# Performance work log

Hardware: AMD Instinct MI355X
Metric: run time of the kernel (lower is better)

Reference implementation:

```python
import jax, jax.numpy as jnp
import numpy as np

B, F, H, M, T = 4096, 256, 256, 3, 30
IN0 = 2 + F  # GRU layer-0 input: concat(current_pos[2], context[F])


def setup_inputs() -> dict:
    key = jax.random.key(0)
    ks = jax.random.split(key, 15)
    s = 0.05
    rn = lambda k, shp: jax.random.normal(k, shp, jnp.float32) * s
    return dict(
        context=jax.random.normal(ks[0], (B, F), jnp.float32),
        mp_w1=rn(ks[1], (64, F)), mp_b1=rn(ks[2], (64,)),
        mp_w2=rn(ks[3], (M, 64)), mp_b2=rn(ks[4], (M,)),
        w_ih0=rn(ks[5], (M, 3 * H, IN0)), w_hh0=rn(ks[6], (M, 3 * H, H)),
        b_ih0=rn(ks[7], (M, 3 * H)), b_hh0=rn(ks[8], (M, 3 * H)),
        w_ih1=rn(ks[9], (M, 3 * H, H)), w_hh1=rn(ks[10], (M, 3 * H, H)),
        b_ih1=rn(ks[11], (M, 3 * H)), b_hh1=rn(ks[12], (M, 3 * H)),
        out_w=rn(ks[13], (M, 2, H)), out_b=rn(ks[14], (M, 2)),
        num_future_steps=T,
    )


def _gru_cell(x, h, w_ih, w_hh, b_ih, b_hh):
    # PyTorch GRU cell, gate order (r, z, n)
    gx = x @ w_ih.T + b_ih  # (B, 3H)
    gh = h @ w_hh.T + b_hh  # (B, 3H)
    xr, xz, xn = jnp.split(gx, 3, axis=-1)
    hr, hz, hn = jnp.split(gh, 3, axis=-1)
    r = jax.nn.sigmoid(xr + hr)
    z = jax.nn.sigmoid(xz + hz)
    n = jnp.tanh(xn + r * hn)
    return (1.0 - z) * n + z * h


def reference(context, mp_w1, mp_b1, mp_w2, mp_b2,
              w_ih0, w_hh0, b_ih0, b_hh0,
              w_ih1, w_hh1, b_ih1, b_hh1,
              out_w, out_b, num_future_steps):
    mode_logits = jax.nn.relu(context @ mp_w1.T + mp_b1) @ mp_w2.T + mp_b2
    mode_probs = jax.nn.softmax(mode_logits, axis=-1)  # (B, M)

    def decode_mode(wi0, wh0, bi0, bh0, wi1, wh1, bi1, bh1, ow, ob):
        def step(carry, _):
            h0, h1, pos = carry
            x = jnp.concatenate([pos, context], axis=-1)  # (B, 2+F)
            h0n = _gru_cell(x, h0, wi0, wh0, bi0, bh0)
            h1n = _gru_cell(h0n, h1, wi1, wh1, bi1, bh1)
            delta = h1n @ ow.T + ob  # (B, 2)
            return (h0n, h1n, delta), delta

        pos0 = jnp.zeros((context.shape[0], 2), context.dtype)
        # hidden = context.unsqueeze(0).repeat(2,1,1): both layers init to context
        (_, _, _), deltas = jax.lax.scan(step, (context, context, pos0), None,
                                          length=num_future_steps)
        # deltas: (T, B, 2) -> (B, T, 2), cumulative sum over time
        return jnp.cumsum(deltas.transpose(1, 0, 2), axis=1)

    trajs = jax.vmap(decode_mode)(w_ih0, w_hh0, b_ih0, b_hh0,
                                  w_ih1, w_hh1, b_ih1, b_hh1,
                                  out_w, out_b)  # (M, B, T, 2)
    trajectories = trajs.transpose(1, 0, 2, 3)  # (B, M, T, 2)
    return trajectories, mode_probs
```

## Files before the change

kernel.cpp:

```cpp
#include <hip/hip_runtime.h>


typedef __attribute__((ext_vector_type(8))) short bf16x8;
typedef __attribute__((ext_vector_type(4))) float f32x4;

__device__ __forceinline__ short f2bf(float f) {
    unsigned u = __builtin_bit_cast(unsigned, f);
    unsigned r = (u + 0x7fffu + ((u >> 16) & 1u)) >> 16;
    return (short)r;
}
__device__ __forceinline__ float bf2f(short s) {
    unsigned u = ((unsigned)(unsigned short)s) << 16;
    return __builtin_bit_cast(float, u);
}
__device__ __forceinline__ float fast_sigmoid(float x) {
    x = fminf(fmaxf(x, -30.f), 30.f);
    float e = __builtin_amdgcn_exp2f(x * -1.442695041f);
    return __builtin_amdgcn_rcpf(1.f + e);
}
__device__ __forceinline__ float fast_tanh(float x) {
    x = fminf(fmaxf(x, -15.f), 15.f);
    float e = __builtin_amdgcn_exp2f(x * -2.885390082f);
    return (1.f - e) * __builtin_amdgcn_rcpf(1.f + e);
}

__global__ void prep_kernel(const float* __restrict__ w_ih0,
                            const float* __restrict__ w_hh0,
                            const float* __restrict__ w_ih1,
                            const float* __restrict__ w_hh1,
                            short* __restrict__ ws) {
    int bid = blockIdx.x;
    int L = threadIdx.x;
    const float* src;
    int srcRowLen, colBase, m, w, ks, t;
    if (bid < 1152) {
        int idx = bid, mw = idx / 48, blk = idx % 48;
        m = mw / 8; w = mw % 8;
        if (blk < 32) { ks = blk >> 2; t = blk & 3; }
        else { int q = blk - 32; ks = q >> 1; t = 4 + (q & 1); }
        src = w_hh0 + (size_t)m * 768 * 256; srcRowLen = 256; colBase = 0;
    } else if (bid < 3456) {
        int idx = bid - 1152, mw = idx / 96, blk = idx % 96;
        m = mw / 8; w = mw % 8;
        int half;
        if (blk < 64) { half = blk >> 5; ks = (blk >> 2) & 7; t = blk & 3; }
        else { int q = blk - 64; half = q >> 4; ks = (q >> 1) & 7; t = 4 + (q & 1); }
        src = (half ? w_hh1 : w_ih1) + (size_t)m * 768 * 256;
        srcRowLen = 256; colBase = 0;
    } else {
        int idx = bid - 3456, mw = idx / 48, blk = idx % 48;
        m = mw / 8; w = mw % 8; ks = blk / 6; t = blk % 6;
        src = w_ih0 + (size_t)m * 768 * 258; srcRowLen = 258; colBase = 2;
    }
    int row = (t >> 1) * 256 + 32 * w + (t & 1) * 16 + (L & 15);
    int col0 = colBase + ks * 32 + (L >> 4) * 8;
    short* dst = ws + (size_t)bid * 512 + L * 8;
    const float* s = src + (size_t)row * srcRowLen + col0;
#pragma unroll
    for (int j = 0; j < 8; ++j) dst[j] = f2bf(s[j]);
}

__global__ __launch_bounds__(256) void modeprobs_kernel(
    const float* __restrict__ ctx, const float* __restrict__ w1,
    const float* __restrict__ b1, const float* __restrict__ w2,
    const float* __restrict__ b2, float* __restrict__ out,
    long probs_off) {
    __shared__ float w1s[64 * 256];
    int tid = threadIdx.x;
    int j = tid & 63;
    int rsub = tid >> 6;
#pragma unroll
    for (int i = 0; i < 64; ++i) w1s[tid + i * 256] = w1[tid + i * 256];
    float b1v = b1[j];
    float w2v0 = w2[j], w2v1 = w2[64 + j], w2v2 = w2[128 + j];
    float b20 = b2[0], b21 = b2[1], b22 = b2[2];
    __syncthreads();
    for (int c = 0; c < 16; ++c) {
        int brow = blockIdx.x * 64 + c * 4 + rsub;
        const float* crow = ctx + (size_t)brow * 256;
        float accv = b1v;
#pragma unroll 8
        for (int k = 0; k < 256; ++k) {
            int kk = (k + j) & 255;
            accv += w1s[j * 256 + kk] * crow[kk];
        }
        float h = fmaxf(accv, 0.f);
        float l0 = h * w2v0, l1 = h * w2v1, l2 = h * w2v2;
#pragma unroll
        for (int s = 1; s < 64; s <<= 1) {
            l0 += __shfl_xor(l0, s);
            l1 += __shfl_xor(l1, s);
            l2 += __shfl_xor(l2, s);
        }
        if (j == 0) {
            l0 += b20; l1 += b21; l2 += b22;
            float mx = fmaxf(l0, fmaxf(l1, l2));
            float e0 = __builtin_amdgcn_exp2f((l0 - mx) * 1.442695041f);
            float e1 = __builtin_amdgcn_exp2f((l1 - mx) * 1.442695041f);
            float e2 = __builtin_amdgcn_exp2f((l2 - mx) * 1.442695041f);
            float inv = 1.f / (e0 + e1 + e2);
            out[probs_off + (size_t)brow * 3 + 0] = e0 * inv;
            out[probs_off + (size_t)brow * 3 + 1] = e1 * inv;
            out[probs_off + (size_t)brow * 3 + 2] = e2 * inv;
        }
    }
}

__global__ __launch_bounds__(512, 2) void decoder_kernel(
    const float* __restrict__ context,
    const float* __restrict__ w_ih0_f,
    const float* __restrict__ b_ih0, const float* __restrict__ b_hh0,
    const float* __restrict__ b_ih1, const float* __restrict__ b_hh1,
    const float* __restrict__ out_w, const float* __restrict__ out_b,
    const short* __restrict__ ws, float* __restrict__ out,
    const int* __restrict__ pT, int ntiles) {
    __shared__ short ctxS[64 * 264];
    __shared__ short h0a[64 * 264], h0b[64 * 264];
    __shared__ short h1s[64 * 264];
    __shared__ float posD[128];
    __shared__ float owl[512];
    __shared__ float cwp0[768], cwp1[768];
    __shared__ float cbA[512];
    __shared__ float cbXn[256];
    __shared__ float cbh0n[256];
    __shared__ float cb1A[512];
    __shared__ float cb1X[256];
    __shared__ float cb1H[256];

    const int bid = blockIdx.x;
    const int xcd = bid & 7, slot = bid >> 3;
    int mode, xl, nx;
    if (xcd < 3)      { mode = 0; xl = xcd;     nx = 3; }
    else if (xcd < 6) { mode = 1; xl = xcd - 3; nx = 3; }
    else              { mode = 2; xl = xcd - 6; nx = 2; }
    const int g = slot * nx + xl;
    if (g >= ntiles) return;
    const int m = mode;
    const int b0 = g * 64;

    const int T = *pT;
    const int tid = threadIdx.x;
    const int lane = tid & 63, w = tid >> 6;
    const int lr = lane & 15, quad = lane >> 4;

    if (tid < 128) posD[tid] = 0.f;
    owl[tid] = out_w[m * 512 + tid];
    if (tid < 512) {
        cbA[tid] = b_ih0[m * 768 + tid] + b_hh0[m * 768 + tid];
        cb1A[tid] = b_ih1[m * 768 + tid] + b_hh1[m * 768 + tid];
    }
    if (tid < 256) {
        cbXn[tid] = b_ih0[m * 768 + 512 + tid];
        cbh0n[tid] = b_hh0[m * 768 + 512 + tid];
        cb1X[tid] = b_ih1[m * 768 + 512 + tid];
        cb1H[tid] = b_hh1[m * 768 + 512 + tid];
    }
    for (int c = tid; c < 768; c += 512) {
        cwp0[c] = w_ih0_f[((size_t)m * 768 + c) * 258 + 0];
        cwp1[c] = w_ih0_f[((size_t)m * 768 + c) * 258 + 1];
    }
#pragma unroll
    for (int i = 0; i < 32; ++i) {
        int idx = tid + i * 512;
        int r = idx >> 8, k = idx & 255;
        short v = f2bf(context[(size_t)(b0 + r) * 256 + k]);
        ctxS[r * 264 + k] = v;
        h0a[r * 264 + k] = v;
        h1s[r * 264 + k] = v;
    }
    const float ob0v = out_b[m * 2 + 0], ob1v = out_b[m * 2 + 1];

    const short* p0w = ws + ((size_t)(m * 8 + w) * 48) * 512 + lane * 8;
    const short* p1w = ws + (size_t)1152 * 512 + ((size_t)(m * 8 + w) * 96) * 512 + lane * 8;
    const short* pcw = ws + (size_t)3456 * 512 + ((size_t)(m * 8 + w) * 48) * 512 + lane * 8;

    const int cA = 32 * w + lr;
    const int cB = 32 * w + 16 + lr;

    __syncthreads();

    float cum0 = 0.f, cum1 = 0.f;

    for (int st = 0; st < T; ++st) {
        const short* h0c = (st & 1) ? h0b : h0a;
        short* h0n_ = (st & 1) ? h0a : h0b;

        {
            f32x4 arz[4][4], axn[2][4], ahn[2][4];
#pragma unroll
            for (int rt = 0; rt < 4; ++rt)
#pragma unroll
                for (int r = 0; r < 4; ++r) {
                    int row = rt * 16 + quad * 4 + r;
                    float px = posD[row * 2], py = posD[row * 2 + 1];
#pragma unroll
                    for (int t = 0; t < 4; ++t) {
                        int c = (t >> 1) * 256 + ((t & 1) ? cB : cA);
                        arz[t][rt][r] = cbA[c] + px * cwp0[c] + py * cwp1[c];
                    }
#pragma unroll
                    for (int nt = 0; nt < 2; ++nt) {
                        int cn = nt ? cB : cA;
                        axn[nt][rt][r] = cbXn[cn] + px * cwp0[512 + cn] +
                                         py * cwp1[512 + cn];
                        ahn[nt][rt][r] = cbh0n[cn];
                    }
                }
            const short* bpc = pcw;
            const short* bp0rz = p0w;
            const short* bp0n = p0w + 32 * 512;
#pragma unroll 1
            for (int ks = 0; ks < 8; ++ks) {
                bf16x8 ac[4], ah[4];
#pragma unroll
                for (int rt = 0; rt < 4; ++rt) {
                    ac[rt] = *reinterpret_cast<const bf16x8*>(
                        ctxS + (rt * 16 + lr) * 264 + ks * 32 + quad * 8);
                    ah[rt] = *reinterpret_cast<const bf16x8*>(
                        h0c + (rt * 16 + lr) * 264 + ks * 32 + quad * 8);
                }
#pragma unroll
                for (int t = 0; t < 4; ++t) {
                    bf16x8 b = *reinterpret_cast<const bf16x8*>(bpc + t * 512);
#pragma unroll
                    for (int rt = 0; rt < 4; ++rt)
                        arz[t][rt] = __builtin_amdgcn_mfma_f32_16x16x32_bf16(
                            ac[rt], b, arz[t][rt], 0, 0, 0);
                }
#pragma unroll
                for (int nt = 0; nt < 2; ++nt) {
                    bf16x8 b = *reinterpret_cast<const bf16x8*>(bpc + (4 + nt) * 512);
#pragma unroll
                    for (int rt = 0; rt < 4; ++rt)
                        axn[nt][rt] = __builtin_amdgcn_mfma_f32_16x16x32_bf16(
                            ac[rt], b, axn[nt][rt], 0, 0, 0);
                }
#pragma unroll
                for (int t = 0; t < 4; ++t) {
                    bf16x8 b = *reinterpret_cast<const bf16x8*>(bp0rz + t * 512);
#pragma unroll
                    for (int rt = 0; rt < 4; ++rt)
                        arz[t][rt] = __builtin_amdgcn_mfma_f32_16x16x32_bf16(
                            ah[rt], b, arz[t][rt], 0, 0, 0);
                }
#pragma unroll
                for (int nt = 0; nt < 2; ++nt) {
                    bf16x8 b = *reinterpret_cast<const bf16x8*>(bp0n + nt * 512);
#pragma unroll
                    for (int rt = 0; rt < 4; ++rt)
                        ahn[nt][rt] = __builtin_amdgcn_mfma_f32_16x16x32_bf16(
                            ah[rt], b, ahn[nt][rt], 0, 0, 0);
                }
                bpc += 6 * 512;
                bp0rz += 4 * 512;
                bp0n += 2 * 512;
            }
#pragma unroll
            for (int nt = 0; nt < 2; ++nt) {
                int col = nt ? cB : cA;
#pragma unroll
                for (int rt = 0; rt < 4; ++rt)
#pragma unroll
                    for (int r = 0; r < 4; ++r) {
                        int row = rt * 16 + quad * 4 + r;
                        float rr = fast_sigmoid(arz[nt][rt][r]);
                        float zz = fast_sigmoid(arz[2 + nt][rt][r]);
                        float nn =
                            fast_tanh(axn[nt][rt][r] + rr * ahn[nt][rt][r]);
                        float hold = bf2f(h0c[row * 264 + col]);
                        h0n_[row * 264 + col] = f2bf((1.f - zz) * nn + zz * hold);
                    }
            }
        }
        __syncthreads();

        {
            f32x4 arz[4][4], axn[2][4], ahn[2][4];
#pragma unroll
            for (int rt = 0; rt < 4; ++rt)
#pragma unroll
                for (int r = 0; r < 4; ++r) {
#pragma unroll
                    for (int t = 0; t < 4; ++t) {
                        int c = (t >> 1) * 256 + ((t & 1) ? cB : cA);
                        arz[t][rt][r] = cb1A[c];
                    }
#pragma unroll
                    for (int nt = 0; nt < 2; ++nt) {
                        int cn = nt ? cB : cA;
                        axn[nt][rt][r] = cb1X[cn];
                        ahn[nt][rt][r] = cb1H[cn];
                    }
                }
            const short* bq0 = p1w;
            const short* bq1 = p1w + 32 * 512;
            const short* bx = p1w + 64 * 512;
            const short* bh = p1w + 80 * 512;
#pragma unroll 1
            for (int ks = 0; ks < 8; ++ks) {
                bf16x8 a0[4], a1[4];
#pragma unroll
                for (int rt = 0; rt < 4; ++rt) {
                    a0[rt] = *reinterpret_cast<const bf16x8*>(
                        h0n_ + (rt * 16 + lr) * 264 + ks * 32 + quad * 8);
                    a1[rt] = *reinterpret_cast<const bf16x8*>(
                        h1s + (rt * 16 + lr) * 264 + ks * 32 + quad * 8);
                }
#pragma unroll
                for (int t = 0; t < 4; ++t) {
                    bf16x8 b = *reinterpret_cast<const bf16x8*>(bq0 + t * 512);
#pragma unroll
                    for (int rt = 0; rt < 4; ++rt)
                        arz[t][rt] = __builtin_amdgcn_mfma_f32_16x16x32_bf16(
                            a0[rt], b, arz[t][rt], 0, 0, 0);
                }
#pragma unroll
                for (int nt = 0; nt < 2; ++nt) {
                    bf16x8 b = *reinterpret_cast<const bf16x8*>(bx + nt * 512);
#pragma unroll
                    for (int rt = 0; rt < 4; ++rt)
                        axn[nt][rt] = __builtin_amdgcn_mfma_f32_16x16x32_bf16(
                            a0[rt], b, axn[nt][rt], 0, 0, 0);
                }
#pragma unroll
                for (int t = 0; t < 4; ++t) {
                    bf16x8 b = *reinterpret_cast<const bf16x8*>(bq1 + t * 512);
#pragma unroll
                    for (int rt = 0; rt < 4; ++rt)
                        arz[t][rt] = __builtin_amdgcn_mfma_f32_16x16x32_bf16(
                            a1[rt], b, arz[t][rt], 0, 0, 0);
                }
#pragma unroll
                for (int nt = 0; nt < 2; ++nt) {
                    bf16x8 b = *reinterpret_cast<const bf16x8*>(bh + nt * 512);
#pragma unroll
                    for (int rt = 0; rt < 4; ++rt)
                        ahn[nt][rt] = __builtin_amdgcn_mfma_f32_16x16x32_bf16(
                            a1[rt], b, ahn[nt][rt], 0, 0, 0);
                }
                bq0 += 4 * 512;
                bq1 += 4 * 512;
                bx += 2 * 512;
                bh += 2 * 512;
            }
            __syncthreads();
#pragma unroll
            for (int nt = 0; nt < 2; ++nt) {
                int col = nt ? cB : cA;
#pragma unroll
                for (int rt = 0; rt < 4; ++rt)
#pragma unroll
                    for (int r = 0; r < 4; ++r) {
                        int row = rt * 16 + quad * 4 + r;
                        float rr = fast_sigmoid(arz[nt][rt][r]);
                        float zz = fast_sigmoid(arz[2 + nt][rt][r]);
                        float nn =
                            fast_tanh(axn[nt][rt][r] + rr * ahn[nt][rt][r]);
                        float hold = bf2f(h1s[row * 264 + col]);
                        h1s[row * 264 + col] = f2bf((1.f - zz) * nn + zz * hold);
                    }
            }
        }
        __syncthreads();

        {
            int brow = tid >> 3, p = tid & 7;
            float d0 = 0.f, d1 = 0.f;
#pragma unroll
            for (int j = 0; j < 4; ++j) {
                int cb = ((p + brow) & 7) * 8 + j * 64;
                bf16x8 hv8 = *reinterpret_cast<const bf16x8*>(h1s + brow * 264 + cb);
#pragma unroll
                for (int i = 0; i < 8; ++i) {
                    float hv = bf2f(hv8[i]);
                    d0 += hv * owl[cb + i];
                    d1 += hv * owl[256 + cb + i];
                }
            }
            d0 += __shfl_xor(d0, 1); d0 += __shfl_xor(d0, 2); d0 += __shfl_xor(d0, 4);
            d1 += __shfl_xor(d1, 1); d1 += __shfl_xor(d1, 2); d1 += __shfl_xor(d1, 4);
            d0 += ob0v;
            d1 += ob1v;
            if (p == 0) {
                cum0 += d0;
                cum1 += d1;
                size_t o = (((size_t)(b0 + brow) * 3 + m) * (size_t)T + st) * 2;
                out[o] = cum0;
                out[o + 1] = cum1;
                posD[brow * 2] = d0;
                posD[brow * 2 + 1] = d1;
            }
        }
        __syncthreads();
    }
}

extern "C" void kernel_launch(void* const* d_in, const int* in_sizes, int n_in,
                              void* d_out, int out_size, void* d_ws, size_t ws_size,
                              hipStream_t stream) {
    const float* context = (const float*)d_in[0];
    const float* mp_w1 = (const float*)d_in[1];
    const float* mp_b1 = (const float*)d_in[2];
    const float* mp_w2 = (const float*)d_in[3];
    const float* mp_b2 = (const float*)d_in[4];
    const float* w_ih0 = (const float*)d_in[5];
    const float* w_hh0 = (const float*)d_in[6];
    const float* b_ih0 = (const float*)d_in[7];
    const float* b_hh0 = (const float*)d_in[8];
    const float* w_ih1 = (const float*)d_in[9];
    const float* w_hh1 = (const float*)d_in[10];
    const float* b_ih1 = (const float*)d_in[11];
    const float* b_hh1 = (const float*)d_in[12];
    const float* out_w = (const float*)d_in[13];
    const float* out_b = (const float*)d_in[14];
    const int* pT = (const int*)d_in[15];
    float* out = (float*)d_out;
    short* ws = (short*)d_ws;

    const int B = in_sizes[0] / 256;
    const int ntiles = B / 64;
    const long probs_off = (long)out_size - (long)B * 3;

    prep_kernel<<<4608, 64, 0, stream>>>(w_ih0, w_hh0, w_ih1, w_hh1, ws);
    modeprobs_kernel<<<B / 64, 256, 0, stream>>>(context, mp_w1, mp_b1, mp_w2,
                                                 mp_b2, out, probs_off);
    const int nslots = (ntiles + 1) / 2;
    decoder_kernel<<<8 * nslots, 512, 0, stream>>>(
        context, w_ih0, b_ih0, b_hh0, b_ih1, b_hh1, out_w, out_b, ws, out, pT,
        ntiles);
}
```

Baseline: 976.4 us.

## Switch GRU recurrent GEMMs from 16x16x32 to 32x32x16 bf16 MFMA tiles

Replaces the 16x16x32 MFMA tiling of both GRU layers with 32x32x16 MFMA, where each wave covers a 32-column slice with two 64-row tiles. The prep kernel re-packs the bf16 weight fragments to match the new operand layout. The gate epilogues and bias initialisation are rewritten for the 32x32 accumulator register mapping. The aim is fewer MFMA instructions and fewer LDS A-operand loads per unit of work, in exchange for a new fragment layout and different register pressure.

```diff
diff --git a/kernel.cpp b/kernel.cpp
--- a/kernel.cpp
+++ b/kernel.cpp
@@ -2,7 +2,7 @@
 
 
 typedef __attribute__((ext_vector_type(8))) short bf16x8;
-typedef __attribute__((ext_vector_type(4))) float f32x4;
+typedef __attribute__((ext_vector_type(16))) float f32x16;
 
 __device__ __forceinline__ short f2bf(float f) {
     unsigned u = __builtin_bit_cast(unsigned, f);
@@ -32,28 +32,32 @@
     int bid = blockIdx.x;
     int L = threadIdx.x;
     const float* src;
-    int srcRowLen, colBase, m, w, ks, t;
+    int srcRowLen, colBase, m, w, ks, gb;
     if (bid < 1152) {
         int idx = bid, mw = idx / 48, blk = idx % 48;
         m = mw / 8; w = mw % 8;
-        if (blk < 32) { ks = blk >> 2; t = blk & 3; }
-        else { int q = blk - 32; ks = q >> 1; t = 4 + (q & 1); }
+        if (blk < 32) { ks = blk >> 1; gb = (blk & 1) * 256; }
+        else { ks = blk - 32; gb = 512; }
         src = w_hh0 + (size_t)m * 768 * 256; srcRowLen = 256; colBase = 0;
     } else if (bid < 3456) {
         int idx = bid - 1152, mw = idx / 96, blk = idx % 96;
         m = mw / 8; w = mw % 8;
         int half;
-        if (blk < 64) { half = blk >> 5; ks = (blk >> 2) & 7; t = blk & 3; }
-        else { int q = blk - 64; half = q >> 4; ks = (q >> 1) & 7; t = 4 + (q & 1); }
+        if (blk < 32)      { half = 0; ks = blk >> 1;        gb = (blk & 1) * 256; }
+        else if (blk < 64) { half = 1; ks = (blk - 32) >> 1; gb = (blk & 1) * 256; }
+        else if (blk < 80) { half = 0; ks = blk - 64;        gb = 512; }
+        else               { half = 1; ks = blk - 80;        gb = 512; }
         src = (half ? w_hh1 : w_ih1) + (size_t)m * 768 * 256;
         srcRowLen = 256; colBase = 0;
     } else {
         int idx = bid - 3456, mw = idx / 48, blk = idx % 48;
-        m = mw / 8; w = mw % 8; ks = blk / 6; t = blk % 6;
+        m = mw / 8; w = mw % 8;
+        if (blk < 32) { ks = blk >> 1; gb = (blk & 1) * 256; }
+        else { ks = blk - 32; gb = 512; }
         src = w_ih0 + (size_t)m * 768 * 258; srcRowLen = 258; colBase = 2;
     }
-    int row = (t >> 1) * 256 + 32 * w + (t & 1) * 16 + (L & 15);
-    int col0 = colBase + ks * 32 + (L >> 4) * 8;
+    int row = gb + 32 * w + (L & 31);
+    int col0 = colBase + ks * 16 + (L >> 5) * 8;
     short* dst = ws + (size_t)bid * 512 + L * 8;
     const float* s = src + (size_t)row * srcRowLen + col0;
 #pragma unroll
@@ -141,7 +145,8 @@
     const int T = *pT;
     const int tid = threadIdx.x;
     const int lane = tid & 63, w = tid >> 6;
-    const int lr = lane & 15, quad = lane >> 4;
+    const int l31 = lane & 31, lhi = lane >> 5;
+    const int c = 32 * w + l31;
 
     if (tid < 128) posD[tid] = 0.f;
     owl[tid] = out_w[m * 512 + tid];
@@ -155,9 +160,9 @@
         cb1X[tid] = b_ih1[m * 768 + 512 + tid];
         cb1H[tid] = b_hh1[m * 768 + 512 + tid];
     }
-    for (int c = tid; c < 768; c += 512) {
-        cwp0[c] = w_ih0_f[((size_t)m * 768 + c) * 258 + 0];
-        cwp1[c] = w_ih0_f[((size_t)m * 768 + c) * 258 + 1];
+    for (int cc = tid; cc < 768; cc += 512) {
+        cwp0[cc] = w_ih0_f[((size_t)m * 768 + cc) * 258 + 0];
+        cwp1[cc] = w_ih0_f[((size_t)m * 768 + cc) * 258 + 1];
     }
 #pragma unroll
     for (int i = 0; i < 32; ++i) {
@@ -174,9 +179,6 @@
     const short* p1w = ws + (size_t)1152 * 512 + ((size_t)(m * 8 + w) * 96) * 512 + lane * 8;
     const short* pcw = ws + (size_t)3456 * 512 + ((size_t)(m * 8 + w) * 48) * 512 + lane * 8;
 
-    const int cA = 32 * w + lr;
-    const int cB = 32 * w + 16 + lr;
-
     __syncthreads();
 
     float cum0 = 0.f, cum1 = 0.f;
@@ -186,180 +188,169 @@
         short* h0n_ = (st & 1) ? h0a : h0b;
 
         {
-            f32x4 arz[4][4], axn[2][4], ahn[2][4];
-#pragma unroll
-            for (int rt = 0; rt < 4; ++rt)
-#pragma unroll
-                for (int r = 0; r < 4; ++r) {
-                    int row = rt * 16 + quad * 4 + r;
-                    float px = posD[row * 2], py = posD[row * 2 + 1];
-#pragma unroll
-                    for (int t = 0; t < 4; ++t) {
-                        int c = (t >> 1) * 256 + ((t & 1) ? cB : cA);
-                        arz[t][rt][r] = cbA[c] + px * cwp0[c] + py * cwp1[c];
+            f32x16 arz[2][2], axn[2], ahn[2];
+            const float bAr = cbA[c], bAz = cbA[256 + c];
+            const float bXnv = cbXn[c], bh0nv = cbh0n[c];
+            const float w0r = cwp0[c], w1r = cwp1[c];
+            const float w0z = cwp0[256 + c], w1z = cwp1[256 + c];
+            const float w0n = cwp0[512 + c], w1n = cwp1[512 + c];
+#pragma unroll
+            for (int rt = 0; rt < 2; ++rt)
+#pragma unroll
+                for (int gq = 0; gq < 4; ++gq)
+#pragma unroll
+                    for (int q = 0; q < 4; ++q) {
+                        int reg = gq * 4 + q;
+                        int row = rt * 32 + q + 8 * gq + 4 * lhi;
+                        float px = posD[row * 2], py = posD[row * 2 + 1];
+                        arz[0][rt][reg] = bAr + px * w0r + py * w1r;
+                        arz[1][rt][reg] = bAz + px * w0z + py * w1z;
+                        axn[rt][reg] = bXnv + px * w0n + py * w1n;
+                        ahn[rt][reg] = bh0nv;
                     }
-#pragma unroll
-                    for (int nt = 0; nt < 2; ++nt) {
-                        int cn = nt ? cB : cA;
-                        axn[nt][rt][r] = cbXn[cn] + px * cwp0[512 + cn] +
-                                         py * cwp1[512 + cn];
-                        ahn[nt][rt][r] = cbh0n[cn];
+            const short* bcr = pcw;
+            const short* bcn = pcw + 32 * 512;
+            const short* b0r = p0w;
+            const short* b0n = p0w + 32 * 512;
+#pragma unroll 1
+            for (int ks = 0; ks < 16; ++ks) {
+                bf16x8 ac[2], ah[2];
+#pragma unroll
+                for (int rt = 0; rt < 2; ++rt) {
+                    ac[rt] = *reinterpret_cast<const bf16x8*>(
+                        ctxS + (rt * 32 + l31) * 264 + ks * 16 + lhi * 8);
+                    ah[rt] = *reinterpret_cast<const bf16x8*>(
+                        h0c + (rt * 32 + l31) * 264 + ks * 16 + lhi * 8);
+                }
+#pragma unroll
+                for (int t = 0; t < 2; ++t) {
+                    bf16x8 b = *reinterpret_cast<const bf16x8*>(bcr + t * 512);
+#pragma unroll
+                    for (int rt = 0; rt < 2; ++rt)
+                        arz[t][rt] = __builtin_amdgcn_mfma_f32_32x32x16_bf16(
+                            ac[rt], b, arz[t][rt], 0, 0, 0);
+                }
+                {
+                    bf16x8 b = *reinterpret_cast<const bf16x8*>(bcn);
+#pragma unroll
+                    for (int rt = 0; rt < 2; ++rt)
+                        axn[rt] = __builtin_amdgcn_mfma_f32_32x32x16_bf16(
+                            ac[rt], b, axn[rt], 0, 0, 0);
+                }
+#pragma unroll
+                for (int t = 0; t < 2; ++t) {
+                    bf16x8 b = *reinterpret_cast<const bf16x8*>(b0r + t * 512);
+#pragma unroll
+                    for (int rt = 0; rt < 2; ++rt)
+                        arz[t][rt] = __builtin_amdgcn_mfma_f32_32x32x16_bf16(
+                            ah[rt], b, arz[t][rt], 0, 0, 0);
+                }
+                {
+                    bf16x8 b = *reinterpret_cast<const bf16x8*>(b0n);
+#pragma unroll
+                    for (int rt = 0; rt < 2; ++rt)
+                        ahn[rt] = __builtin_amdgcn_mfma_f32_32x32x16_bf16(
+                            ah[rt], b, ahn[rt], 0, 0, 0);
+                }
+                bcr += 2 * 512;
+                bcn += 512;
+                b0r += 2 * 512;
+                b0n += 512;
+            }
+#pragma unroll
+            for (int rt = 0; rt < 2; ++rt)
+#pragma unroll
+                for (int gq = 0; gq < 4; ++gq)
+#pragma unroll
+                    for (int q = 0; q < 4; ++q) {
+                        int reg = gq * 4 + q;
+                        int row = rt * 32 + q + 8 * gq + 4 * lhi;
+                        float rr = fast_sigmoid(arz[0][rt][reg]);
+                        float zz = fast_sigmoid(arz[1][rt][reg]);
+                        float nn = fast_tanh(axn[rt][reg] + rr * ahn[rt][reg]);
+                        float hold = bf2f(h0c[row * 264 + c]);
+                        h0n_[row * 264 + c] = f2bf((1.f - zz) * nn + zz * hold);
                     }
-                }
-            const short* bpc = pcw;
-            const short* bp0rz = p0w;
-            const short* bp0n = p0w + 32 * 512;
-#pragma unroll 1
-            for (int ks = 0; ks < 8; ++ks) {
-                bf16x8 ac[4], ah[4];
-#pragma unroll
-                for (int rt = 0; rt < 4; ++rt) {
-                    ac[rt] = *reinterpret_cast<const bf16x8*>(
-                        ctxS + (rt * 16 + lr) * 264 + ks * 32 + quad * 8);
-                    ah[rt] = *reinterpret_cast<const bf16x8*>(
-                        h0c + (rt * 16 + lr) * 264 + ks * 32 + quad * 8);
-                }
-#pragma unroll
-                for (int t = 0; t < 4; ++t) {
-                    bf16x8 b = *reinterpret_cast<const bf16x8*>(bpc + t * 512);
-#pragma unroll
-                    for (int rt = 0; rt < 4; ++rt)
-                        arz[t][rt] = __builtin_amdgcn_mfma_f32_16x16x32_bf16(
-                            ac[rt], b, arz[t][rt], 0, 0, 0);
-                }
-#pragma unroll
-                for (int nt = 0; nt < 2; ++nt) {
-                    bf16x8 b = *reinterpret_cast<const bf16x8*>(bpc + (4 + nt) * 512);
-#pragma unroll
-                    for (int rt = 0; rt < 4; ++rt)
-                        axn[nt][rt] = __builtin_amdgcn_mfma_f32_16x16x32_bf16(
-                            ac[rt], b, axn[nt][rt], 0, 0, 0);
-                }
-#pragma unroll
-                for (int t = 0; t < 4; ++t) {
-                    bf16x8 b = *reinterpret_cast<const bf16x8*>(bp0rz + t * 512);
-#pragma unroll
-                    for (int rt = 0; rt < 4; ++rt)
-                        arz[t][rt] = __builtin_amdgcn_mfma_f32_16x16x32_bf16(
-                            ah[rt], b, arz[t][rt], 0, 0, 0);
-                }
-#pragma unroll
-                for (int nt = 0; nt < 2; ++nt) {
-                    bf16x8 b = *reinterpret_cast<const bf16x8*>(bp0n + nt * 512);
-#pragma unroll
-                    for (int rt = 0; rt < 4; ++rt)
-                        ahn[nt][rt] = __builtin_amdgcn_mfma_f32_16x16x32_bf16(
-                            ah[rt], b, ahn[nt][rt], 0, 0, 0);
-                }
-                bpc += 6 * 512;
-                bp0rz += 4 * 512;
-                bp0n += 2 * 512;
-            }
-#pragma unroll
-            for (int nt = 0; nt < 2; ++nt) {
-                int col = nt ? cB : cA;
-#pragma unroll
-                for (int rt = 0; rt < 4; ++rt)
-#pragma unroll
-                    for (int r = 0; r < 4; ++r) {
-                        int row = rt * 16 + quad * 4 + r;
-                        float rr = fast_sigmoid(arz[nt][rt][r]);
-                        float zz = fast_sigmoid(arz[2 + nt][rt][r]);
-                        float nn =
-                            fast_tanh(axn[nt][rt][r] + rr * ahn[nt][rt][r]);
-                        float hold = bf2f(h0c[row * 264 + col]);
-                        h0n_[row * 264 + col] = f2bf((1.f - zz) * nn + zz * hold);
-                    }
-            }
         }
         __syncthreads();
 
         {
-            f32x4 arz[4][4], axn[2][4], ahn[2][4];
-#pragma unroll
-            for (int rt = 0; rt < 4; ++rt)
-#pragma unroll
-                for (int r = 0; r < 4; ++r) {
-#pragma unroll
-                    for (int t = 0; t < 4; ++t) {
-                        int c = (t >> 1) * 256 + ((t & 1) ? cB : cA);
-                        arz[t][rt][r] = cb1A[c];
-                    }
-#pragma unroll
-                    for (int nt = 0; nt < 2; ++nt) {
-                        int cn = nt ? cB : cA;
-                        axn[nt][rt][r] = cb1X[cn];
-                        ahn[nt][rt][r] = cb1H[cn];
-                    }
+            f32x16 arz[2][2], axn[2], ahn[2];
+            const float bAr = cb1A[c], bAz = cb1A[256 + c];
+            const float bXv = cb1X[c], bHv = cb1H[c];
+#pragma unroll
+            for (int rt = 0; rt < 2; ++rt)
+#pragma unroll
+                for (int reg = 0; reg < 16; ++reg) {
+                    arz[0][rt][reg] = bAr;
+                    arz[1][rt][reg] = bAz;
+                    axn[rt][reg] = bXv;
+                    ahn[rt][reg] = bHv;
                 }
             const short* bq0 = p1w;
             const short* bq1 = p1w + 32 * 512;
             const short* bx = p1w + 64 * 512;
             const short* bh = p1w + 80 * 512;
 #pragma unroll 1
-            for (int ks = 0; ks < 8; ++ks) {
-                bf16x8 a0[4], a1[4];
-#pragma unroll
-                for (int rt = 0; rt < 4; ++rt) {
+            for (int ks = 0; ks < 16; ++ks) {
+                bf16x8 a0[2], a1[2];
+#pragma unroll
+                for (int rt = 0; rt < 2; ++rt) {
                     a0[rt] = *reinterpret_cast<const bf16x8*>(
-                        h0n_ + (rt * 16 + lr) * 264 + ks * 32 + quad * 8);
+                        h0n_ + (rt * 32 + l31) * 264 + ks * 16 + lhi * 8);
                     a1[rt] = *reinterpret_cast<const bf16x8*>(
-                        h1s + (rt * 16 + lr) * 264 + ks * 32 + quad * 8);
-                }
-#pragma unroll
-                for (int t = 0; t < 4; ++t) {
+                        h1s + (rt * 32 + l31) * 264 + ks * 16 + lhi * 8);
+                }
+#pragma unroll
+                for (int t = 0; t < 2; ++t) {
                     bf16x8 b = *reinterpret_cast<const bf16x8*>(bq0 + t * 512);
 #pragma unroll
-                    for (int rt = 0; rt < 4; ++rt)
-                        arz[t][rt] = __builtin_amdgcn_mfma_f32_16x16x32_bf16(
+                    for (int rt = 0; rt < 2; ++rt)
+                        arz[t][rt] = __builtin_amdgcn_mfma_f32_32x32x16_bf16(
                             a0[rt], b, arz[t][rt], 0, 0, 0);
                 }
-#pragma unroll
-                for (int nt = 0; nt < 2; ++nt) {
-                    bf16x8 b = *reinterpret_cast<const bf16x8*>(bx + nt * 512);
-#pragma unroll
-                    for (int rt = 0; rt < 4; ++rt)
-                        axn[nt][rt] = __builtin_amdgcn_mfma_f32_16x16x32_bf16(
-                            a0[rt], b, axn[nt][rt], 0, 0, 0);
-                }
-#pragma unroll
-                for (int t = 0; t < 4; ++t) {
+                {
+                    bf16x8 b = *reinterpret_cast<const bf16x8*>(bx);
+#pragma unroll
+                    for (int rt = 0; rt < 2; ++rt)
+                        axn[rt] = __builtin_amdgcn_mfma_f32_32x32x16_bf16(
+                            a0[rt], b, axn[rt], 0, 0, 0);
+                }
+#pragma unroll
+                for (int t = 0; t < 2; ++t) {
                     bf16x8 b = *reinterpret_cast<const bf16x8*>(bq1 + t * 512);
 #pragma unroll
-                    for (int rt = 0; rt < 4; ++rt)
-                        arz[t][rt] = __builtin_amdgcn_mfma_f32_16x16x32_bf16(
+                    for (int rt = 0; rt < 2; ++rt)
+                        arz[t][rt] = __builtin_amdgcn_mfma_f32_32x32x16_bf16(
                             a1[rt], b, arz[t][rt], 0, 0, 0);
                 }
-#pragma unroll
-                for (int nt = 0; nt < 2; ++nt) {
-                    bf16x8 b = *reinterpret_cast<const bf16x8*>(bh + nt * 512);
-#pragma unroll
-                    for (int rt = 0; rt < 4; ++rt)
-                        ahn[nt][rt] = __builtin_amdgcn_mfma_f32_16x16x32_bf16(
-                            a1[rt], b, ahn[nt][rt], 0, 0, 0);
-                }
-                bq0 += 4 * 512;
-                bq1 += 4 * 512;
-                bx += 2 * 512;
-                bh += 2 * 512;
+                {
+                    bf16x8 b = *reinterpret_cast<const bf16x8*>(bh);
+#pragma unroll
+                    for (int rt = 0; rt < 2; ++rt)
+                        ahn[rt] = __builtin_amdgcn_mfma_f32_32x32x16_bf16(
+                            a1[rt], b, ahn[rt], 0, 0, 0);
+                }
+                bq0 += 2 * 512;
+                bq1 += 2 * 512;
+                bx += 512;
+                bh += 512;
             }
             __syncthreads();
 #pragma unroll
-            for (int nt = 0; nt < 2; ++nt) {
-                int col = nt ? cB : cA;
-#pragma unroll
-                for (int rt = 0; rt < 4; ++rt)
-#pragma unroll
-                    for (int r = 0; r < 4; ++r) {
-                        int row = rt * 16 + quad * 4 + r;
-                        float rr = fast_sigmoid(arz[nt][rt][r]);
-                        float zz = fast_sigmoid(arz[2 + nt][rt][r]);
-                        float nn =
-                            fast_tanh(axn[nt][rt][r] + rr * ahn[nt][rt][r]);
-                        float hold = bf2f(h1s[row * 264 + col]);
-                        h1s[row * 264 + col] = f2bf((1.f - zz) * nn + zz * hold);
+            for (int rt = 0; rt < 2; ++rt)
+#pragma unroll
+                for (int gq = 0; gq < 4; ++gq)
+#pragma unroll
+                    for (int q = 0; q < 4; ++q) {
+                        int reg = gq * 4 + q;
+                        int row = rt * 32 + q + 8 * gq + 4 * lhi;
+                        float rr = fast_sigmoid(arz[0][rt][reg]);
+                        float zz = fast_sigmoid(arz[1][rt][reg]);
+                        float nn = fast_tanh(axn[rt][reg] + rr * ahn[rt][reg]);
+                        float hold = bf2f(h1s[row * 264 + c]);
+                        h1s[row * 264 + c] = f2bf((1.f - zz) * nn + zz * hold);
                     }
-            }
         }
         __syncthreads();
 
```

Measured after the change: 1.113 ms. 1.14x slower.

## Halve decoder tile to 32 rows with 256-thread blocks and rebalanced work map

Applied to the files above, without the earlier changes.

The decoder now processes 32-row batch tiles with 4 waves per block instead of 64 rows with 8 waves. Each wave covers two 32-column groups, so per-wave weight loads are reused across fewer rows. Work items are spread across the mode/tile space with a per-XCD contiguous split instead of the fixed 3/3/2 mode-to-XCD mapping. The pos-projection weights are stored in shared memory as bf16. The goal is more blocks and better occupancy and load balance across CUs, at the cost of each weight fragment read from global/L2 being reused over half as many rows, which raises weight traffic.

```diff
diff --git a/kernel.cpp b/kernel.cpp
--- a/kernel.cpp
+++ b/kernel.cpp
@@ -106,20 +106,20 @@
     }
 }
 
-__global__ __launch_bounds__(512, 2) void decoder_kernel(
+__global__ __launch_bounds__(256, 2) void decoder_kernel(
     const float* __restrict__ context,
     const float* __restrict__ w_ih0_f,
     const float* __restrict__ b_ih0, const float* __restrict__ b_hh0,
     const float* __restrict__ b_ih1, const float* __restrict__ b_hh1,
     const float* __restrict__ out_w, const float* __restrict__ out_b,
     const short* __restrict__ ws, float* __restrict__ out,
-    const int* __restrict__ pT, int ntiles) {
-    __shared__ short ctxS[64 * 264];
-    __shared__ short h0a[64 * 264], h0b[64 * 264];
-    __shared__ short h1s[64 * 264];
-    __shared__ float posD[128];
+    const int* __restrict__ pT, int tilesPerMode, int nwork) {
+    __shared__ short ctxS[32 * 264];
+    __shared__ short h0a[32 * 264], h0b[32 * 264];
+    __shared__ short h1s[32 * 264];
+    __shared__ float posD[64];
     __shared__ float owl[512];
-    __shared__ float cwp0[768], cwp1[768];
+    __shared__ short cwp0h[768], cwp1h[768];
     __shared__ float cbA[512];
     __shared__ float cbXn[256];
     __shared__ float cbh0n[256];
@@ -127,55 +127,57 @@
     __shared__ float cb1X[256];
     __shared__ float cb1H[256];
 
-    const int bid = blockIdx.x;
-    const int xcd = bid & 7, slot = bid >> 3;
-    int mode, xl, nx;
-    if (xcd < 3)      { mode = 0; xl = xcd;     nx = 3; }
-    else if (xcd < 6) { mode = 1; xl = xcd - 3; nx = 3; }
-    else              { mode = 2; xl = xcd - 6; nx = 2; }
-    const int g = slot * nx + xl;
-    if (g >= ntiles) return;
-    const int m = mode;
-    const int b0 = g * 64;
+    const int lane8 = blockIdx.x & 7, slot = blockIdx.x >> 3;
+    const int q = nwork >> 3, r8 = nwork & 7;
+    int start, cnt;
+    if (lane8 < r8) { cnt = q + 1; start = lane8 * (q + 1); }
+    else            { cnt = q;     start = r8 * (q + 1) + (lane8 - r8) * q; }
+    if (slot >= cnt) return;
+    const int work = start + slot;
+    const int m = work / tilesPerMode;
+    const int b0 = (work - m * tilesPerMode) * 32;
 
     const int T = *pT;
     const int tid = threadIdx.x;
     const int lane = tid & 63, w = tid >> 6;
     const int lr = lane & 15, quad = lane >> 4;
 
-    if (tid < 128) posD[tid] = 0.f;
+    if (tid < 64) posD[tid] = 0.f;
     owl[tid] = out_w[m * 512 + tid];
-    if (tid < 512) {
-        cbA[tid] = b_ih0[m * 768 + tid] + b_hh0[m * 768 + tid];
-        cb1A[tid] = b_ih1[m * 768 + tid] + b_hh1[m * 768 + tid];
-    }
-    if (tid < 256) {
-        cbXn[tid] = b_ih0[m * 768 + 512 + tid];
-        cbh0n[tid] = b_hh0[m * 768 + 512 + tid];
-        cb1X[tid] = b_ih1[m * 768 + 512 + tid];
-        cb1H[tid] = b_hh1[m * 768 + 512 + tid];
-    }
-    for (int c = tid; c < 768; c += 512) {
-        cwp0[c] = w_ih0_f[((size_t)m * 768 + c) * 258 + 0];
-        cwp1[c] = w_ih0_f[((size_t)m * 768 + c) * 258 + 1];
+    owl[256 + tid] = out_w[m * 512 + 256 + tid];
+    cbA[tid] = b_ih0[m * 768 + tid] + b_hh0[m * 768 + tid];
+    cbA[256 + tid] = b_ih0[m * 768 + 256 + tid] + b_hh0[m * 768 + 256 + tid];
+    cb1A[tid] = b_ih1[m * 768 + tid] + b_hh1[m * 768 + tid];
+    cb1A[256 + tid] = b_ih1[m * 768 + 256 + tid] + b_hh1[m * 768 + 256 + tid];
+    cbXn[tid] = b_ih0[m * 768 + 512 + tid];
+    cbh0n[tid] = b_hh0[m * 768 + 512 + tid];
+    cb1X[tid] = b_ih1[m * 768 + 512 + tid];
+    cb1H[tid] = b_hh1[m * 768 + 512 + tid];
+    for (int cc = tid; cc < 768; cc += 256) {
+        cwp0h[cc] = f2bf(w_ih0_f[((size_t)m * 768 + cc) * 258 + 0]);
+        cwp1h[cc] = f2bf(w_ih0_f[((size_t)m * 768 + cc) * 258 + 1]);
     }
 #pragma unroll
     for (int i = 0; i < 32; ++i) {
-        int idx = tid + i * 512;
-        int r = idx >> 8, k = idx & 255;
-        short v = f2bf(context[(size_t)(b0 + r) * 256 + k]);
-        ctxS[r * 264 + k] = v;
-        h0a[r * 264 + k] = v;
-        h1s[r * 264 + k] = v;
+        int idx = tid + i * 256;
+        int rr = idx >> 8, k = idx & 255;
+        short v = f2bf(context[(size_t)(b0 + rr) * 256 + k]);
+        ctxS[rr * 264 + k] = v;
+        h0a[rr * 264 + k] = v;
+        h1s[rr * 264 + k] = v;
     }
     const float ob0v = out_b[m * 2 + 0], ob1v = out_b[m * 2 + 1];
 
-    const short* p0w = ws + ((size_t)(m * 8 + w) * 48) * 512 + lane * 8;
-    const short* p1w = ws + (size_t)1152 * 512 + ((size_t)(m * 8 + w) * 96) * 512 + lane * 8;
-    const short* pcw = ws + (size_t)3456 * 512 + ((size_t)(m * 8 + w) * 48) * 512 + lane * 8;
-
-    const int cA = 32 * w + lr;
-    const int cB = 32 * w + 16 + lr;
+    const short* p0B[2];
+    const short* p1B[2];
+    const short* pcB[2];
+#pragma unroll
+    for (int g2 = 0; g2 < 2; ++g2) {
+        const int wg = 2 * w + g2;
+        p0B[g2] = ws + ((size_t)(m * 8 + wg) * 48) * 512 + lane * 8;
+        p1B[g2] = ws + (size_t)1152 * 512 + ((size_t)(m * 8 + wg) * 96) * 512 + lane * 8;
+        pcB[g2] = ws + (size_t)3456 * 512 + ((size_t)(m * 8 + wg) * 48) * 512 + lane * 8;
+    }
 
     __syncthreads();
 
@@ -186,180 +188,237 @@
         short* h0n_ = (st & 1) ? h0a : h0b;
 
         {
-            f32x4 arz[4][4], axn[2][4], ahn[2][4];
-#pragma unroll
-            for (int rt = 0; rt < 4; ++rt)
-#pragma unroll
-                for (int r = 0; r < 4; ++r) {
-                    int row = rt * 16 + quad * 4 + r;
-                    float px = posD[row * 2], py = posD[row * 2 + 1];
-#pragma unroll
-                    for (int t = 0; t < 4; ++t) {
-                        int c = (t >> 1) * 256 + ((t & 1) ? cB : cA);
-                        arz[t][rt][r] = cbA[c] + px * cwp0[c] + py * cwp1[c];
-                    }
-#pragma unroll
-                    for (int nt = 0; nt < 2; ++nt) {
-                        int cn = nt ? cB : cA;
-                        axn[nt][rt][r] = cbXn[cn] + px * cwp0[512 + cn] +
-                                         py * cwp1[512 + cn];
-                        ahn[nt][rt][r] = cbh0n[cn];
-                    }
-                }
-            const short* bpc = pcw;
-            const short* bp0rz = p0w;
-            const short* bp0n = p0w + 32 * 512;
+            f32x4 arz[2][4][2], axn[2][2][2], ahn[2][2][2];
+            float px[2][4], py[2][4];
+#pragma unroll
+            for (int rt = 0; rt < 2; ++rt)
+#pragma unroll
+                for (int rr = 0; rr < 4; ++rr) {
+                    int row = rt * 16 + quad * 4 + rr;
+                    px[rt][rr] = posD[row * 2];
+                    py[rt][rr] = posD[row * 2 + 1];
+                }
+#pragma unroll
+            for (int g2 = 0; g2 < 2; ++g2) {
+                const int cbase = 32 * (2 * w + g2) + lr;
+#pragma unroll
+                for (int t = 0; t < 4; ++t) {
+                    const int c = (t >> 1) * 256 + cbase + (t & 1) * 16;
+                    const float bb = cbA[c];
+                    const float w0 = bf2f(cwp0h[c]), w1 = bf2f(cwp1h[c]);
+#pragma unroll
+                    for (int rt = 0; rt < 2; ++rt)
+#pragma unroll
+                        for (int rr = 0; rr < 4; ++rr)
+                            arz[g2][t][rt][rr] =
+                                bb + px[rt][rr] * w0 + py[rt][rr] * w1;
+                }
+#pragma unroll
+                for (int nt = 0; nt < 2; ++nt) {
+                    const int cn = cbase + nt * 16;
+                    const float bx = cbXn[cn], bh = cbh0n[cn];
+                    const float w0 = bf2f(cwp0h[512 + cn]);
+                    const float w1 = bf2f(cwp1h[512 + cn]);
+#pragma unroll
+                    for (int rt = 0; rt < 2; ++rt)
+#pragma unroll
+                        for (int rr = 0; rr < 4; ++rr) {
+                            axn[g2][nt][rt][rr] =
+                                bx + px[rt][rr] * w0 + py[rt][rr] * w1;
+                            ahn[g2][nt][rt][rr] = bh;
+                        }
+                }
+            }
+            const short* bpc0 = pcB[0];
+            const short* bpc1 = pcB[1];
+            const short* brz0 = p0B[0];
+            const short* brz1 = p0B[1];
+            const short* bn0 = p0B[0] + 32 * 512;
+            const short* bn1 = p0B[1] + 32 * 512;
 #pragma unroll 1
             for (int ks = 0; ks < 8; ++ks) {
-                bf16x8 ac[4], ah[4];
-#pragma unroll
-                for (int rt = 0; rt < 4; ++rt) {
+                bf16x8 ac[2], ah[2];
+#pragma unroll
+                for (int rt = 0; rt < 2; ++rt) {
                     ac[rt] = *reinterpret_cast<const bf16x8*>(
                         ctxS + (rt * 16 + lr) * 264 + ks * 32 + quad * 8);
                     ah[rt] = *reinterpret_cast<const bf16x8*>(
                         h0c + (rt * 16 + lr) * 264 + ks * 32 + quad * 8);
                 }
 #pragma unroll
+                for (int g2 = 0; g2 < 2; ++g2) {
+                    const short* bpc = g2 ? bpc1 : bpc0;
+                    const short* brz = g2 ? brz1 : brz0;
+                    const short* bn = g2 ? bn1 : bn0;
+#pragma unroll
+                    for (int t = 0; t < 4; ++t) {
+                        bf16x8 b = *reinterpret_cast<const bf16x8*>(bpc + t * 512);
+#pragma unroll
+                        for (int rt = 0; rt < 2; ++rt)
+                            arz[g2][t][rt] = __builtin_amdgcn_mfma_f32_16x16x32_bf16(
+                                ac[rt], b, arz[g2][t][rt], 0, 0, 0);
+                    }
+#pragma unroll
+                    for (int nt = 0; nt < 2; ++nt) {
+                        bf16x8 b = *reinterpret_cast<const bf16x8*>(bpc + (4 + nt) * 512);
+#pragma unroll
+                        for (int rt = 0; rt < 2; ++rt)
+                            axn[g2][nt][rt] = __builtin_amdgcn_mfma_f32_16x16x32_bf16(
+                                ac[rt], b, axn[g2][nt][rt], 0, 0, 0);
+                    }
+#pragma unroll
+                    for (int t = 0; t < 4; ++t) {
+                        bf16x8 b = *reinterpret_cast<const bf16x8*>(brz + t * 512);
+#pragma unroll
+                        for (int rt = 0; rt < 2; ++rt)
+                            arz[g2][t][rt] = __builtin_amdgcn_mfma_f32_16x16x32_bf16(
+                                ah[rt], b, arz[g2][t][rt], 0, 0, 0);
+                    }
+#pragma unroll
+                    for (int nt = 0; nt < 2; ++nt) {
+                        bf16x8 b = *reinterpret_cast<const bf16x8*>(bn + nt * 512);
+#pragma unroll
+                        for (int rt = 0; rt < 2; ++rt)
+                            ahn[g2][nt][rt] = __builtin_amdgcn_mfma_f32_16x16x32_bf16(
+                                ah[rt], b, ahn[g2][nt][rt], 0, 0, 0);
+                    }
+                }
+                bpc0 += 6 * 512; bpc1 += 6 * 512;
+                brz0 += 4 * 512; brz1 += 4 * 512;
+                bn0 += 2 * 512;  bn1 += 2 * 512;
+            }
+#pragma unroll
+            for (int g2 = 0; g2 < 2; ++g2)
+#pragma unroll
+                for (int nt = 0; nt < 2; ++nt) {
+                    const int col = 32 * (2 * w + g2) + nt * 16 + lr;
+#pragma unroll
+                    for (int rt = 0; rt < 2; ++rt)
+#pragma unroll
+                        for (int rr = 0; rr < 4; ++rr) {
+                            int row = rt * 16 + quad * 4 + rr;
+                            float rg = fast_sigmoid(arz[g2][nt][rt][rr]);
+                            float zg = fast_sigmoid(arz[g2][2 + nt][rt][rr]);
+                            float ng = fast_tanh(axn[g2][nt][rt][rr] +
+                                                 rg * ahn[g2][nt][rt][rr]);
+                            float hold = bf2f(h0c[row * 264 + col]);
+                            h0n_[row * 264 + col] =
+                                f2bf((1.f - zg) * ng + zg * hold);
+                        }
+                }
+        }
+        __syncthreads();
+
+        {
+            f32x4 arz[2][4][2], axn[2][2][2], ahn[2][2][2];
+#pragma unroll
+            for (int g2 = 0; g2 < 2; ++g2) {
+                const int cbase = 32 * (2 * w + g2) + lr;
+#pragma unroll
                 for (int t = 0; t < 4; ++t) {
-                    bf16x8 b = *reinterpret_cast<const bf16x8*>(bpc + t * 512);
-#pragma unroll
-                    for (int rt = 0; rt < 4; ++rt)
-                        arz[t][rt] = __builtin_amdgcn_mfma_f32_16x16x32_bf16(
-                            ac[rt], b, arz[t][rt], 0, 0, 0);
+                    const int c = (t >> 1) * 256 + cbase + (t & 1) * 16;
+                    const float bb = cb1A[c];
+#pragma unroll
+                    for (int rt = 0; rt < 2; ++rt)
+#pragma unroll
+                        for (int rr = 0; rr < 4; ++rr)
+                            arz[g2][t][rt][rr] = bb;
                 }
 #pragma unroll
                 for (int nt = 0; nt < 2; ++nt) {
-                    bf16x8 b = *reinterpret_cast<const bf16x8*>(bpc + (4 + nt) * 512);
-#pragma unroll
-                    for (int rt = 0; rt < 4; ++rt)
-                        axn[nt][rt] = __builtin_amdgcn_mfma_f32_16x16x32_bf16(
-                            ac[rt], b, axn[nt][rt], 0, 0, 0);
-                }
-#pragma unroll
-                for (int t = 0; t < 4; ++t) {
-                    bf16x8 b = *reinterpret_cast<const bf16x8*>(bp0rz + t * 512);
-#pragma unroll
-                    for (int rt = 0; rt < 4; ++rt)
-                        arz[t][rt] = __builtin_amdgcn_mfma_f32_16x16x32_bf16(
-                            ah[rt], b, arz[t][rt], 0, 0, 0);
-                }
-#pragma unroll
-                for (int nt = 0; nt < 2; ++nt) {
-                    bf16x8 b = *reinterpret_cast<const bf16x8*>(bp0n + nt * 512);
-#pragma unroll
-                    for (int rt = 0; rt < 4; ++rt)
-                        ahn[nt][rt] = __builtin_amdgcn_mfma_f32_16x16x32_bf16(
-                            ah[rt], b, ahn[nt][rt], 0, 0, 0);
-                }
-                bpc += 6 * 512;
-                bp0rz += 4 * 512;
-                bp0n += 2 * 512;
-            }
-#pragma unroll
-            for (int nt = 0; nt < 2; ++nt) {
-                int col = nt ? cB : cA;
-#pragma unroll
-                for (int rt = 0; rt < 4; ++rt)
-#pragma unroll
-                    for (int r = 0; r < 4; ++r) {
-                        int row = rt * 16 + quad * 4 + r;
-                        float rr = fast_sigmoid(arz[nt][rt][r]);
-                        float zz = fast_sigmoid(arz[2 + nt][rt][r]);
-                        float nn =
-                            fast_tanh(axn[nt][rt][r] + rr * ahn[nt][rt][r]);
-                        float hold = bf2f(h0c[row * 264 + col]);
-                        h0n_[row * 264 + col] = f2bf((1.f - zz) * nn + zz * hold);
-                    }
-            }
-        }
-        __syncthreads();
-
-        {
-            f32x4 arz[4][4], axn[2][4], ahn[2][4];
-#pragma unroll
-            for (int rt = 0; rt < 4; ++rt)
-#pragma unroll
-                for (int r = 0; r < 4; ++r) {
-#pragma unroll
-                    for (int t = 0; t < 4; ++t) {
-                        int c = (t >> 1) * 256 + ((t & 1) ? cB : cA);
-                        arz[t][rt][r] = cb1A[c];
-                    }
-#pragma unroll
-                    for (int nt = 0; nt < 2; ++nt) {
-                        int cn = nt ? cB : cA;
-                        axn[nt][rt][r] = cb1X[cn];
-                        ahn[nt][rt][r] = cb1H[cn];
-                    }
-                }
-            const short* bq0 = p1w;
-            const short* bq1 = p1w + 32 * 512;
-            const short* bx = p1w + 64 * 512;
-            const short* bh = p1w + 80 * 512;
+                    const int cn = cbase + nt * 16;
+                    const float bx = cb1X[cn], bh = cb1H[cn];
+#pragma unroll
+                    for (int rt = 0; rt < 2; ++rt)
+#pragma unroll
+                        for (int rr = 0; rr < 4; ++rr) {
+                            axn[g2][nt][rt][rr] = bx;
+                            ahn[g2][nt][rt][rr] = bh;
+                        }
+                }
+            }
+            const short* bq00 = p1B[0];
+            const short* bq01 = p1B[1];
+            const short* bq10 = p1B[0] + 32 * 512;
+            const short* bq11 = p1B[1] + 32 * 512;
+            const short* bx0 = p1B[0] + 64 * 512;
+            const short* bx1 = p1B[1] + 64 * 512;
+            const short* bh0 = p1B[0] + 80 * 512;
+            const short* bh1 = p1B[1] + 80 * 512;
 #pragma unroll 1
             for (int ks = 0; ks < 8; ++ks) {
-                bf16x8 a0[4], a1[4];
-#pragma unroll
-                for (int rt = 0; rt < 4; ++rt) {
+                bf16x8 a0[2], a1[2];
+#pragma unroll
+                for (int rt = 0; rt < 2; ++rt) {
                     a0[rt] = *reinterpret_cast<const bf16x8*>(
                         h0n_ + (rt * 16 + lr) * 264 + ks * 32 + quad * 8);
                     a1[rt] = *reinterpret_cast<const bf16x8*>(
                         h1s + (rt * 16 + lr) * 264 + ks * 32 + quad * 8);
                 }
 #pragma unroll
-                for (int t = 0; t < 4; ++t) {
-                    bf16x8 b = *reinterpret_cast<const bf16x8*>(bq0 + t * 512);
-#pragma unroll
-                    for (int rt = 0; rt < 4; ++rt)
-                        arz[t][rt] = __builtin_amdgcn_mfma_f32_16x16x32_bf16(
-                            a0[rt], b, arz[t][rt], 0, 0, 0);
-                }
+                for (int g2 = 0; g2 < 2; ++g2) {
+                    const short* bq0 = g2 ? bq01 : bq00;
+                    const short* bq1 = g2 ? bq11 : bq10;
+                    const short* bxp = g2 ? bx1 : bx0;
+                    const short* bhp = g2 ? bh1 : bh0;
+#pragma unroll
+                    for (int t = 0; t < 4; ++t) {
+                        bf16x8 b = *reinterpret_cast<const bf16x8*>(bq0 + t * 512);
+#pragma unroll
+                        for (int rt = 0; rt < 2; ++rt)
+                            arz[g2][t][rt] = __builtin_amdgcn_mfma_f32_16x16x32_bf16(
+                                a0[rt], b, arz[g2][t][rt], 0, 0, 0);
+                    }
+#pragma unroll
+                    for (int nt = 0; nt < 2; ++nt) {
+                        bf16x8 b = *reinterpret_cast<const bf16x8*>(bxp + nt * 512);
+#pragma unroll
+                        for (int rt = 0; rt < 2; ++rt)
+                            axn[g2][nt][rt] = __builtin_amdgcn_mfma_f32_16x16x32_bf16(
+                                a0[rt], b, axn[g2][nt][rt], 0, 0, 0);
+                    }
+#pragma unroll
+                    for (int t = 0; t < 4; ++t) {
+                        bf16x8 b = *reinterpret_cast<const bf16x8*>(bq1 + t * 512);
+#pragma unroll
+                        for (int rt = 0; rt < 2; ++rt)
+                            arz[g2][t][rt] = __builtin_amdgcn_mfma_f32_16x16x32_bf16(
+                                a1[rt], b, arz[g2][t][rt], 0, 0, 0);
+                    }
+#pragma unroll
+                    for (int nt = 0; nt < 2; ++nt) {
+                        bf16x8 b = *reinterpret_cast<const bf16x8*>(bhp + nt * 512);
+#pragma unroll
+                        for (int rt = 0; rt < 2; ++rt)
+                            ahn[g2][nt][rt] = __builtin_amdgcn_mfma_f32_16x16x32_bf16(
+                                a1[rt], b, ahn[g2][nt][rt], 0, 0, 0);
+                    }
+                }
+                bq00 += 4 * 512; bq01 += 4 * 512;
+                bq10 += 4 * 512; bq11 += 4 * 512;
+                bx0 += 2 * 512;  bx1 += 2 * 512;
+                bh0 += 2 * 512;  bh1 += 2 * 512;
+            }
+            __syncthreads();
+#pragma unroll
+            for (int g2 = 0; g2 < 2; ++g2)
 #pragma unroll
                 for (int nt = 0; nt < 2; ++nt) {
-                    bf16x8 b = *reinterpret_cast<const bf16x8*>(bx + nt * 512);
-#pragma unroll
-                    for (int rt = 0; rt < 4; ++rt)
-                        axn[nt][rt] = __builtin_amdgcn_mfma_f32_16x16x32_bf16(
-                            a0[rt], b, axn[nt][rt], 0, 0, 0);
-                }
-#pragma unroll
-                for (int t = 0; t < 4; ++t) {
-                    bf16x8 b = *reinterpret_cast<const bf16x8*>(bq1 + t * 512);
-#pragma unroll
-                    for (int rt = 0; rt < 4; ++rt)
-                        arz[t][rt] = __builtin_amdgcn_mfma_f32_16x16x32_bf16(
-                            a1[rt], b, arz[t][rt], 0, 0, 0);
-                }
-#pragma unroll
-                for (int nt = 0; nt < 2; ++nt) {
-                    bf16x8 b = *reinterpret_cast<const bf16x8*>(bh + nt * 512);
-#pragma unroll
-                    for (int rt = 0; rt < 4; ++rt)
-                        ahn[nt][rt] = __builtin_amdgcn_mfma_f32_16x16x32_bf16(
-                            a1[rt], b, ahn[nt][rt], 0, 0, 0);
-                }
-                bq0 += 4 * 512;
-                bq1 += 4 * 512;
-                bx += 2 * 512;
-                bh += 2 * 512;
-            }
-            __syncthreads();
-#pragma unroll
-            for (int nt = 0; nt < 2; ++nt) {
-                int col = nt ? cB : cA;
-#pragma unroll
-                for (int rt = 0; rt < 4; ++rt)
-#pragma unroll
-                    for (int r = 0; r < 4; ++r) {
-                        int row = rt * 16 + quad * 4 + r;
-                        float rr = fast_sigmoid(arz[nt][rt][r]);
-                        float zz = fast_sigmoid(arz[2 + nt][rt][r]);
-                        float nn =
-                            fast_tanh(axn[nt][rt][r] + rr * ahn[nt][rt][r]);
-                        float hold = bf2f(h1s[row * 264 + col]);
-                        h1s[row * 264 + col] = f2bf((1.f - zz) * nn + zz * hold);
-                    }
-            }
+                    const int col = 32 * (2 * w + g2) + nt * 16 + lr;
+#pragma unroll
+                    for (int rt = 0; rt < 2; ++rt)
+#pragma unroll
+                        for (int rr = 0; rr < 4; ++rr) {
+                            int row = rt * 16 + quad * 4 + rr;
+                            float rg = fast_sigmoid(arz[g2][nt][rt][rr]);
+                            float zg = fast_sigmoid(arz[g2][2 + nt][rt][rr]);
+                            float ng = fast_tanh(axn[g2][nt][rt][rr] +
+                                                 rg * ahn[g2][nt][rt][rr]);
+                            float hold = bf2f(h1s[row * 264 + col]);
+                            h1s[row * 264 + col] =
+                                f2bf((1.f - zg) * ng + zg * hold);
+                        }
+                }
         }
         __syncthreads();
 
@@ -418,14 +477,15 @@
     short* ws = (short*)d_ws;
 
     const int B = in_sizes[0] / 256;
-    const int ntiles = B / 64;
+    const int tilesPerMode = B / 32;
+    const int nwork = 3 * tilesPerMode;
     const long probs_off = (long)out_size - (long)B * 3;
 
     prep_kernel<<<4608, 64, 0, stream>>>(w_ih0, w_hh0, w_ih1, w_hh1, ws);
     modeprobs_kernel<<<B / 64, 256, 0, stream>>>(context, mp_w1, mp_b1, mp_w2,
                                                  mp_b2, out, probs_off);
-    const int nslots = (ntiles + 1) / 2;
-    decoder_kernel<<<8 * nslots, 512, 0, stream>>>(
+    const int grid = 8 * ((nwork + 7) / 8);
+    decoder_kernel<<<grid, 256, 0, stream>>>(
         context, w_ih0, b_ih0, b_hh0, b_ih1, b_hh1, out_w, out_b, ws, out, pT,
-        ntiles);
-}
+        tilesPerMode, nwork);
+}
```

Result: slower. 1.333 ms (+36.5%).
